# Kernel tuning notes

Measured on AMD Instinct MI355X. Metric: run time of the kernel, lower is better.

## Reference

```python
import jax, jax.numpy as jnp
import numpy as np

B, T, D = 2, 512, 512
UNITS, H = 512, 8
DEPTH = UNITS // H  # 64


def setup_inputs() -> dict:
    key = jax.random.key(0)
    ks = jax.random.split(key, 16)
    s = 0.05  # keras 'random_normal' initializer stddev
    inp = {
        "query": jax.random.normal(ks[0], (B, T, D), jnp.float32),
        "key": jax.random.normal(ks[1], (B, T, D), jnp.float32),
        "value": jax.random.normal(ks[2], (B, T, D), jnp.float32),
        # input projections (Dense(units) with bias)
        "Wq": jax.random.normal(ks[3], (D, UNITS), jnp.float32) * s,
        "bq": jnp.zeros((UNITS,), jnp.float32),
        "Wk": jax.random.normal(ks[4], (D, UNITS), jnp.float32) * s,
        "bk": jnp.zeros((UNITS,), jnp.float32),
        "Wv": jax.random.normal(ks[5], (D, UNITS), jnp.float32) * s,
        "bv": jnp.zeros((UNITS,), jnp.float32),
        # per-head additive-attention params, stacked over heads
        "Wq_h": jax.random.normal(ks[6], (H, DEPTH, DEPTH), jnp.float32) * s,
        "Wk_h": jax.random.normal(ks[7], (H, DEPTH, DEPTH), jnp.float32) * s,
        "va_h": jax.random.normal(ks[8], (H, DEPTH), jnp.float32) * s,
        "b_h": jnp.zeros((H, DEPTH), jnp.float32),
        # output projection
        "Wo": jax.random.normal(ks[9], (UNITS, UNITS), jnp.float32) * s,
        "bo": jnp.zeros((UNITS,), jnp.float32),
    }
    return inp


def _split_heads(x):
    b = x.shape[0]
    return x.reshape(b, -1, H, DEPTH).transpose(0, 2, 1, 3)  # [B,H,T,depth]


def reference(query, key, value, Wq, bq, Wk, bk, Wv, bv,
              Wq_h, Wk_h, va_h, b_h, Wo, bo):
    Q = _split_heads(query @ Wq + bq)  # [B,H,T,d]
    K = _split_heads(key @ Wk + bk)    # [B,H,S,d]
    V = _split_heads(value @ Wv + bv)  # computed but unused, as in original

    # per-head linear maps for additive scores
    q = jnp.einsum("bhtd,hde->bhte", Q, Wq_h)
    k = jnp.einsum("bhsd,hde->bhse", K, Wk_h)
    # Bahdanau additive score: tanh(q_t + k_s + b) . v_a, summed over depth
    feat = jnp.tanh(q[:, :, :, None, :] + k[:, :, None, :, :]
                    + b_h[None, :, None, None, :])  # [B,H,T,S,d]
    score = jnp.einsum("bhtse,he->bhts", feat, va_h)  # [B,H,T,S]
    attn = jax.nn.softmax(score, axis=-1)
    # original multiplies by KEY (not value)
    heads = jnp.einsum("bhts,bhsd->bhtd", attn, K)  # [B,H,T,d]
    merged = heads.transpose(0, 2, 1, 3).reshape(query.shape[0], -1, UNITS)
    return merged @ Wo + bo
```

## Files before the change

### kernel.cpp

```cpp
#include <hip/hip_runtime.h>
#include <hip/hip_bf16.h>

#define T_SEQ 512
#define NH 8
#define DEPTH 64
#define UNITS_ 512
#define SCALE2 2.8853900817779268f
#define LOG2E 1.4426950408889634f

typedef __attribute__((ext_vector_type(8))) short short8;
typedef __attribute__((ext_vector_type(4))) float floatx4;

__global__ __launch_bounds__(256) void qk_head_fused(
    const float* __restrict__ query, const float* __restrict__ key,
    const float* __restrict__ Wq, const float* __restrict__ bq,
    const float* __restrict__ Wk, const float* __restrict__ bk,
    const float* __restrict__ Wq_h, const float* __restrict__ Wk_h,
    const float* __restrict__ bh,
    float* __restrict__ eq, float* __restrict__ ekT,
    __hip_bfloat16* __restrict__ KhT)
{
    __shared__ float S1[64][68];
    __shared__ float S2[64][68];

    const int tid = threadIdx.x;
    const int which = blockIdx.z;
    const int h  = blockIdx.x;
    const int m0 = blockIdx.y * 64;
    const int n0 = h * 64;
    const int b  = m0 >> 9;
    const int t0 = m0 & 511;
    const int bh_i = b * NH + h;

    const float* In   = which ? key : query;
    const float* W    = which ? Wk  : Wq;
    const float* bias = which ? bk  : bq;
    const float* Wp   = (which ? Wk_h : Wq_h) + h * 4096;

    float (*As)[68] = S1;
    float (*Bs)[68] = S2;

    const int arow = tid >> 2;
    const int acol = (tid & 3) * 8;
    const int bkk = tid >> 3;
    const int bn = (tid & 7) * 8;

    const int ti = tid >> 4;
    const int tj = tid & 15;

    const int wrow = tid >> 2;
    const int wcol = (tid & 3) * 16;
    float4 wh0 = *(const float4*)&Wp[wrow * 64 + wcol + 0];
    float4 wh1 = *(const float4*)&Wp[wrow * 64 + wcol + 4];
    float4 wh2 = *(const float4*)&Wp[wrow * 64 + wcol + 8];
    float4 wh3 = *(const float4*)&Wp[wrow * 64 + wcol + 12];

    float4 acc[4];
    acc[0] = acc[1] = acc[2] = acc[3] = make_float4(0.f, 0.f, 0.f, 0.f);

    float4 av0 = *(const float4*)&In[(m0 + arow) * 512 + acol];
    float4 av1 = *(const float4*)&In[(m0 + arow) * 512 + acol + 4];
    float4 bv0 = *(const float4*)&W[bkk * 512 + n0 + bn];
    float4 bv1 = *(const float4*)&W[bkk * 512 + n0 + bn + 4];

    for (int k0 = 0; k0 < 512; k0 += 32) {
        __syncthreads();
        As[acol + 0][arow] = av0.x;
        As[acol + 1][arow] = av0.y;
        As[acol + 2][arow] = av0.z;
        As[acol + 3][arow] = av0.w;
        As[acol + 4][arow] = av1.x;
        As[acol + 5][arow] = av1.y;
        As[acol + 6][arow] = av1.z;
        As[acol + 7][arow] = av1.w;
        *(float4*)&Bs[bkk][bn] = bv0;
        *(float4*)&Bs[bkk][bn + 4] = bv1;
        __syncthreads();
        if (k0 + 32 < 512) {
            av0 = *(const float4*)&In[(m0 + arow) * 512 + k0 + 32 + acol];
            av1 = *(const float4*)&In[(m0 + arow) * 512 + k0 + 32 + acol + 4];
            bv0 = *(const float4*)&W[(k0 + 32 + bkk) * 512 + n0 + bn];
            bv1 = *(const float4*)&W[(k0 + 32 + bkk) * 512 + n0 + bn + 4];
        }
        #pragma unroll
        for (int kk = 0; kk < 32; ++kk) {
            float4 a4 = *(const float4*)&As[kk][4 * ti];
            float4 b4 = *(const float4*)&Bs[kk][4 * tj];
            acc[0].x = fmaf(a4.x, b4.x, acc[0].x);
            acc[0].y = fmaf(a4.x, b4.y, acc[0].y);
            acc[0].z = fmaf(a4.x, b4.z, acc[0].z);
            acc[0].w = fmaf(a4.x, b4.w, acc[0].w);
            acc[1].x = fmaf(a4.y, b4.x, acc[1].x);
            acc[1].y = fmaf(a4.y, b4.y, acc[1].y);
            acc[1].z = fmaf(a4.y, b4.z, acc[1].z);
            acc[1].w = fmaf(a4.y, b4.w, acc[1].w);
            acc[2].x = fmaf(a4.z, b4.x, acc[2].x);
            acc[2].y = fmaf(a4.z, b4.y, acc[2].y);
            acc[2].z = fmaf(a4.z, b4.z, acc[2].z);
            acc[2].w = fmaf(a4.z, b4.w, acc[2].w);
            acc[3].x = fmaf(a4.w, b4.x, acc[3].x);
            acc[3].y = fmaf(a4.w, b4.y, acc[3].y);
            acc[3].z = fmaf(a4.w, b4.z, acc[3].z);
            acc[3].w = fmaf(a4.w, b4.w, acc[3].w);
        }
    }

    float4 bb = *(const float4*)&bias[n0 + 4 * tj];
    __syncthreads();
    *(float4*)&S1[4 * tj + 0][4 * ti] =
        make_float4(acc[0].x + bb.x, acc[1].x + bb.x, acc[2].x + bb.x, acc[3].x + bb.x);
    *(float4*)&S1[4 * tj + 1][4 * ti] =
        make_float4(acc[0].y + bb.y, acc[1].y + bb.y, acc[2].y + bb.y, acc[3].y + bb.y);
    *(float4*)&S1[4 * tj + 2][4 * ti] =
        make_float4(acc[0].z + bb.z, acc[1].z + bb.z, acc[2].z + bb.z, acc[3].z + bb.z);
    *(float4*)&S1[4 * tj + 3][4 * ti] =
        make_float4(acc[0].w + bb.w, acc[1].w + bb.w, acc[2].w + bb.w, acc[3].w + bb.w);
    *(float4*)&S2[wrow][wcol + 0]  = wh0;
    *(float4*)&S2[wrow][wcol + 4]  = wh1;
    *(float4*)&S2[wrow][wcol + 8]  = wh2;
    *(float4*)&S2[wrow][wcol + 12] = wh3;
    __syncthreads();

    float4 qa[4];
    qa[0] = qa[1] = qa[2] = qa[3] = make_float4(0.f, 0.f, 0.f, 0.f);
    #pragma unroll 8
    for (int d = 0; d < 64; ++d) {
        float4 a4 = *(const float4*)&S1[d][4 * ti];
        float4 b4 = *(const float4*)&S2[d][4 * tj];
        qa[0].x = fmaf(a4.x, b4.x, qa[0].x);
        qa[0].y = fmaf(a4.x, b4.y, qa[0].y);
        qa[0].z = fmaf(a4.x, b4.z, qa[0].z);
        qa[0].w = fmaf(a4.x, b4.w, qa[0].w);
        qa[1].x = fmaf(a4.y, b4.x, qa[1].x);
        qa[1].y = fmaf(a4.y, b4.y, qa[1].y);
        qa[1].z = fmaf(a4.y, b4.z, qa[1].z);
        qa[1].w = fmaf(a4.y, b4.w, qa[1].w);
        qa[2].x = fmaf(a4.z, b4.x, qa[2].x);
        qa[2].y = fmaf(a4.z, b4.y, qa[2].y);
        qa[2].z = fmaf(a4.z, b4.z, qa[2].z);
        qa[2].w = fmaf(a4.z, b4.w, qa[2].w);
        qa[3].x = fmaf(a4.w, b4.x, qa[3].x);
        qa[3].y = fmaf(a4.w, b4.y, qa[3].y);
        qa[3].z = fmaf(a4.w, b4.z, qa[3].z);
        qa[3].w = fmaf(a4.w, b4.w, qa[3].w);
    }

    if (which == 0) {
        float* outp = eq + ((size_t)bh_i * 512 + t0) * 64;
        #pragma unroll
        for (int r = 0; r < 4; ++r) {
            float4 o;
            o.x = __builtin_amdgcn_exp2f(SCALE2 * qa[r].x);
            o.y = __builtin_amdgcn_exp2f(SCALE2 * qa[r].y);
            o.z = __builtin_amdgcn_exp2f(SCALE2 * qa[r].z);
            o.w = __builtin_amdgcn_exp2f(SCALE2 * qa[r].w);
            *(float4*)&outp[(4 * ti + r) * 64 + 4 * tj] = o;
        }
        return;
    }

    float4 bhv = *(const float4*)&bh[h * 64 + 4 * tj];
    __syncthreads();
    #pragma unroll
    for (int r = 0; r < 4; ++r) {
        S2[4 * tj + 0][4 * ti + r] = __builtin_amdgcn_exp2f(SCALE2 * (qa[r].x + bhv.x));
        S2[4 * tj + 1][4 * ti + r] = __builtin_amdgcn_exp2f(SCALE2 * (qa[r].y + bhv.y));
        S2[4 * tj + 2][4 * ti + r] = __builtin_amdgcn_exp2f(SCALE2 * (qa[r].z + bhv.z));
        S2[4 * tj + 3][4 * ti + r] = __builtin_amdgcn_exp2f(SCALE2 * (qa[r].w + bhv.w));
    }
    __syncthreads();

    const int dd = tid >> 2;
    const int sc = (tid & 3) * 16;
    float* ekp = ekT + ((size_t)bh_i * 64 + dd) * 512 + t0 + sc;
    #pragma unroll
    for (int c = 0; c < 4; ++c)
        *(float4*)&ekp[4 * c] = *(float4*)&S2[dd][sc + 4 * c];

    __hip_bfloat16* kp = KhT + ((size_t)bh_i * 64 + dd) * 512 + t0 + sc;
    union { short8 v; short s[8]; } pk0, pk1;
    #pragma unroll
    for (int i = 0; i < 8; ++i) {
        __hip_bfloat16 b0 = __hip_bfloat16(S1[dd][sc + i]);
        __hip_bfloat16 b1 = __hip_bfloat16(S1[dd][sc + 8 + i]);
        pk0.s[i] = *(short*)&b0;
        pk1.s[i] = *(short*)&b1;
    }
    *(short8*)kp = pk0.v;
    *(short8*)(kp + 8) = pk1.v;
}

__global__ __launch_bounds__(512, 4) void attn_v2(
    const float* __restrict__ eq, const float* __restrict__ ekT,
    const __hip_bfloat16* __restrict__ KhT, const float* __restrict__ va_h,
    float* __restrict__ merged)
{
    __shared__ __hip_bfloat16 pA[16][520];
    __shared__ float wsum[16][8];

    const int tid = threadIdx.x;
    const int w = tid >> 6;
    const int l = tid & 63;
    const int t0 = blockIdx.x * 16;
    const int h = blockIdx.y;
    const int b = blockIdx.z;
    const int bh_i = b * NH + h;

    const float* eq_p = eq + ((size_t)bh_i * 512 + t0) * 64;
    const float* ekT_p = ekT + (size_t)bh_i * 64 * 512 + tid;
    const float* va_p = va_h + h * 64;

    float acc[16];
    #pragma unroll
    for (int t = 0; t < 16; ++t) acc[t] = 0.f;

    #pragma unroll
    for (int e0 = 0; e0 < 64; e0 += 16) {
        float ekv[16];
        #pragma unroll
        for (int j = 0; j < 16; ++j) ekv[j] = ekT_p[(e0 + j) * 512];
        float nv[16];
        #pragma unroll
        for (int j = 0; j < 16; ++j) nv[j] = -2.0f * va_p[e0 + j];
        #pragma unroll
        for (int t = 0; t < 16; ++t) {
            float a = acc[t];
            #pragma unroll
            for (int q = 0; q < 4; ++q) {
                float4 e4 = *(const float4*)&eq_p[t * 64 + e0 + q * 4];
                a = fmaf(nv[q * 4 + 0], __builtin_amdgcn_rcpf(fmaf(e4.x, ekv[q * 4 + 0], 1.0f)), a);
                a = fmaf(nv[q * 4 + 1], __builtin_amdgcn_rcpf(fmaf(e4.y, ekv[q * 4 + 1], 1.0f)), a);
                a = fmaf(nv[q * 4 + 2], __builtin_amdgcn_rcpf(fmaf(e4.z, ekv[q * 4 + 2], 1.0f)), a);
                a = fmaf(nv[q * 4 + 3], __builtin_amdgcn_rcpf(fmaf(e4.w, ekv[q * 4 + 3], 1.0f)), a);
            }
            acc[t] = a;
        }
    }

    float ev[16];
    #pragma unroll
    for (int t = 0; t < 16; ++t) {
        float s = __builtin_amdgcn_exp2f(acc[t] * LOG2E);
        ev[t] = s;
        #pragma unroll
        for (int off = 32; off > 0; off >>= 1) s += __shfl_xor(s, off, 64);
        if (l == 0) wsum[t][w] = s;
    }
    __syncthreads();
    #pragma unroll
    for (int t = 0; t < 16; ++t) {
        float4 s0 = *(float4*)&wsum[t][0];
        float4 s1 = *(float4*)&wsum[t][4];
        float inv = 1.0f / (((s0.x + s0.y) + (s0.z + s0.w)) + ((s1.x + s1.y) + (s1.z + s1.w)));
        pA[t][tid] = __hip_bfloat16(ev[t] * inv);
    }
    __syncthreads();

    if (w < 4) {
        const __hip_bfloat16* kp = KhT + (size_t)bh_i * 64 * 512
                                   + ((size_t)(w * 16 + (l & 15))) * 512 + (l >> 4) * 8;
        const __hip_bfloat16* ap = &pA[l & 15][(l >> 4) * 8];
        floatx4 oacc = {0.f, 0.f, 0.f, 0.f};
        #pragma unroll
        for (int kt = 0; kt < 16; ++kt) {
            short8 af = *(const short8*)(ap + kt * 32);
            short8 bf = *(const short8*)(kp + kt * 32);
            oacc = __builtin_amdgcn_mfma_f32_16x16x32_bf16(af, bf, oacc, 0, 0, 0);
        }
        const int row = (l >> 4) * 4;
        const int col = w * 16 + (l & 15);
        float* mp = merged + ((size_t)(b * 512 + t0 + row)) * 512 + h * 64 + col;
        #pragma unroll
        for (int r = 0; r < 4; ++r) mp[r * 512] = oacc[r];
    }
}

__global__ __launch_bounds__(256) void gemm_out(
    const float* __restrict__ A, const float* __restrict__ W,
    const float* __restrict__ bias, float* __restrict__ C)
{
    __shared__ float As[32][36];
    __shared__ float Bs[32][68];

    const int tid = threadIdx.x;
    const int n0 = blockIdx.x * 64;
    const int m0 = blockIdx.y * 32;

    const int arow = tid >> 3;
    const int acol = (tid & 7) * 4;
    const int bkk = tid >> 3;
    const int bn = (tid & 7) * 8;

    const int ti = tid >> 4;
    const int tj = tid & 15;

    float4 acc0 = make_float4(0.f, 0.f, 0.f, 0.f);
    float4 acc1 = make_float4(0.f, 0.f, 0.f, 0.f);

    float4 av  = *(const float4*)&A[(m0 + arow) * 512 + acol];
    float4 bv0 = *(const float4*)&W[bkk * 512 + n0 + bn];
    float4 bv1 = *(const float4*)&W[bkk * 512 + n0 + bn + 4];

    for (int k0 = 0; k0 < 512; k0 += 32) {
        __syncthreads();
        As[acol + 0][arow] = av.x;
        As[acol + 1][arow] = av.y;
        As[acol + 2][arow] = av.z;
        As[acol + 3][arow] = av.w;
        *(float4*)&Bs[bkk][bn] = bv0;
        *(float4*)&Bs[bkk][bn + 4] = bv1;
        __syncthreads();
        if (k0 + 32 < 512) {
            av  = *(const float4*)&A[(m0 + arow) * 512 + k0 + 32 + acol];
            bv0 = *(const float4*)&W[(k0 + 32 + bkk) * 512 + n0 + bn];
            bv1 = *(const float4*)&W[(k0 + 32 + bkk) * 512 + n0 + bn + 4];
        }
        #pragma unroll
        for (int kk = 0; kk < 32; ++kk) {
            float2 a2 = *(const float2*)&As[kk][2 * ti];
            float4 b4 = *(const float4*)&Bs[kk][4 * tj];
            acc0.x = fmaf(a2.x, b4.x, acc0.x);
            acc0.y = fmaf(a2.x, b4.y, acc0.y);
            acc0.z = fmaf(a2.x, b4.z, acc0.z);
            acc0.w = fmaf(a2.x, b4.w, acc0.w);
            acc1.x = fmaf(a2.y, b4.x, acc1.x);
            acc1.y = fmaf(a2.y, b4.y, acc1.y);
            acc1.z = fmaf(a2.y, b4.z, acc1.z);
            acc1.w = fmaf(a2.y, b4.w, acc1.w);
        }
    }
    float4 bb = *(const float4*)&bias[n0 + 4 * tj];
    float4 o0, o1;
    o0.x = acc0.x + bb.x; o0.y = acc0.y + bb.y; o0.z = acc0.z + bb.z; o0.w = acc0.w + bb.w;
    o1.x = acc1.x + bb.x; o1.y = acc1.y + bb.y; o1.z = acc1.z + bb.z; o1.w = acc1.w + bb.w;
    *(float4*)&C[(m0 + 2 * ti) * 512 + n0 + 4 * tj] = o0;
    *(float4*)&C[(m0 + 2 * ti + 1) * 512 + n0 + 4 * tj] = o1;
}

extern "C" void kernel_launch(void* const* d_in, const int* in_sizes, int n_in,
                              void* d_out, int out_size, void* d_ws, size_t ws_size,
                              hipStream_t stream) {
    (void)in_sizes; (void)n_in; (void)out_size; (void)ws_size;
    const float* query = (const float*)d_in[0];
    const float* key   = (const float*)d_in[1];
    const float* Wq   = (const float*)d_in[3];
    const float* bq   = (const float*)d_in[4];
    const float* Wk   = (const float*)d_in[5];
    const float* bk   = (const float*)d_in[6];
    const float* Wq_h = (const float*)d_in[9];
    const float* Wk_h = (const float*)d_in[10];
    const float* va_h = (const float*)d_in[11];
    const float* b_h  = (const float*)d_in[12];
    const float* Wo   = (const float*)d_in[13];
    const float* bo   = (const float*)d_in[14];

    float* out = (float*)d_out;
    float* ws = (float*)d_ws;
    const int SZ = 1024 * 512;
    float* eqb     = ws;
    float* ekTb    = eqb + SZ;
    float* mergedb = ekTb + SZ;
    __hip_bfloat16* KhTb = (__hip_bfloat16*)(mergedb + SZ);

    qk_head_fused<<<dim3(8, 16, 2), 256, 0, stream>>>(query, key, Wq, bq, Wk, bk,
                                                      Wq_h, Wk_h, b_h,
                                                      eqb, ekTb, KhTb);
    attn_v2<<<dim3(32, 8, 2), 512, 0, stream>>>(eqb, ekTb, KhTb, va_h, mergedb);
    gemm_out<<<dim3(8, 32, 1), 256, 0, stream>>>(mergedb, Wo, bo, out);
}
```

Measured before the change: 181.8 us.

## Halve tile sizes across all three kernels to launch more blocks

Halves the row tile in the fused QK projection kernel (64 to 32 rows), the query tile in the attention kernel (16 to 8 rows, with a 1D swizzled grid over batch-heads and zero-padded MFMA rows), and the output-column tile in the output GEMM. The aim is to raise block counts so the many CUs on the device are filled, since the earlier grids launched only 256 to 512 blocks. The cost is lower per-thread data reuse, more redundant weight loads, and MFMA work wasted on the padded rows in attention.

```diff
diff --git a/kernel.cpp b/kernel.cpp
--- a/kernel.cpp
+++ b/kernel.cpp
@@ -20,13 +20,13 @@
     float* __restrict__ eq, float* __restrict__ ekT,
     __hip_bfloat16* __restrict__ KhT)
 {
-    __shared__ float S1[64][68];
+    __shared__ float S1[64][36];
     __shared__ float S2[64][68];
 
     const int tid = threadIdx.x;
     const int which = blockIdx.z;
     const int h  = blockIdx.x;
-    const int m0 = blockIdx.y * 64;
+    const int m0 = blockIdx.y * 32;
     const int n0 = h * 64;
     const int b  = m0 >> 9;
     const int t0 = m0 & 511;
@@ -37,11 +37,8 @@
     const float* bias = which ? bk  : bq;
     const float* Wp   = (which ? Wk_h : Wq_h) + h * 4096;
 
-    float (*As)[68] = S1;
-    float (*Bs)[68] = S2;
-
-    const int arow = tid >> 2;
-    const int acol = (tid & 3) * 8;
+    const int arow = tid >> 3;
+    const int acol = (tid & 7) * 4;
     const int bkk = tid >> 3;
     const int bn = (tid & 7) * 8;
 
@@ -55,164 +52,148 @@
     float4 wh2 = *(const float4*)&Wp[wrow * 64 + wcol + 8];
     float4 wh3 = *(const float4*)&Wp[wrow * 64 + wcol + 12];
 
-    float4 acc[4];
-    acc[0] = acc[1] = acc[2] = acc[3] = make_float4(0.f, 0.f, 0.f, 0.f);
-
-    float4 av0 = *(const float4*)&In[(m0 + arow) * 512 + acol];
-    float4 av1 = *(const float4*)&In[(m0 + arow) * 512 + acol + 4];
+    float4 acc0 = make_float4(0.f, 0.f, 0.f, 0.f);
+    float4 acc1 = make_float4(0.f, 0.f, 0.f, 0.f);
+
+    float4 av  = *(const float4*)&In[(m0 + arow) * 512 + acol];
     float4 bv0 = *(const float4*)&W[bkk * 512 + n0 + bn];
     float4 bv1 = *(const float4*)&W[bkk * 512 + n0 + bn + 4];
 
     for (int k0 = 0; k0 < 512; k0 += 32) {
         __syncthreads();
-        As[acol + 0][arow] = av0.x;
-        As[acol + 1][arow] = av0.y;
-        As[acol + 2][arow] = av0.z;
-        As[acol + 3][arow] = av0.w;
-        As[acol + 4][arow] = av1.x;
-        As[acol + 5][arow] = av1.y;
-        As[acol + 6][arow] = av1.z;
-        As[acol + 7][arow] = av1.w;
-        *(float4*)&Bs[bkk][bn] = bv0;
-        *(float4*)&Bs[bkk][bn + 4] = bv1;
+        S1[acol + 0][arow] = av.x;
+        S1[acol + 1][arow] = av.y;
+        S1[acol + 2][arow] = av.z;
+        S1[acol + 3][arow] = av.w;
+        *(float4*)&S2[bkk][bn] = bv0;
+        *(float4*)&S2[bkk][bn + 4] = bv1;
         __syncthreads();
         if (k0 + 32 < 512) {
-            av0 = *(const float4*)&In[(m0 + arow) * 512 + k0 + 32 + acol];
-            av1 = *(const float4*)&In[(m0 + arow) * 512 + k0 + 32 + acol + 4];
+            av  = *(const float4*)&In[(m0 + arow) * 512 + k0 + 32 + acol];
             bv0 = *(const float4*)&W[(k0 + 32 + bkk) * 512 + n0 + bn];
             bv1 = *(const float4*)&W[(k0 + 32 + bkk) * 512 + n0 + bn + 4];
         }
         #pragma unroll
         for (int kk = 0; kk < 32; ++kk) {
-            float4 a4 = *(const float4*)&As[kk][4 * ti];
-            float4 b4 = *(const float4*)&Bs[kk][4 * tj];
-            acc[0].x = fmaf(a4.x, b4.x, acc[0].x);
-            acc[0].y = fmaf(a4.x, b4.y, acc[0].y);
-            acc[0].z = fmaf(a4.x, b4.z, acc[0].z);
-            acc[0].w = fmaf(a4.x, b4.w, acc[0].w);
-            acc[1].x = fmaf(a4.y, b4.x, acc[1].x);
-            acc[1].y = fmaf(a4.y, b4.y, acc[1].y);
-            acc[1].z = fmaf(a4.y, b4.z, acc[1].z);
-            acc[1].w = fmaf(a4.y, b4.w, acc[1].w);
-            acc[2].x = fmaf(a4.z, b4.x, acc[2].x);
-            acc[2].y = fmaf(a4.z, b4.y, acc[2].y);
-            acc[2].z = fmaf(a4.z, b4.z, acc[2].z);
-            acc[2].w = fmaf(a4.z, b4.w, acc[2].w);
-            acc[3].x = fmaf(a4.w, b4.x, acc[3].x);
-            acc[3].y = fmaf(a4.w, b4.y, acc[3].y);
-            acc[3].z = fmaf(a4.w, b4.z, acc[3].z);
-            acc[3].w = fmaf(a4.w, b4.w, acc[3].w);
+            float2 a2 = *(const float2*)&S1[kk][2 * ti];
+            float4 b4 = *(const float4*)&S2[kk][4 * tj];
+            acc0.x = fmaf(a2.x, b4.x, acc0.x);
+            acc0.y = fmaf(a2.x, b4.y, acc0.y);
+            acc0.z = fmaf(a2.x, b4.z, acc0.z);
+            acc0.w = fmaf(a2.x, b4.w, acc0.w);
+            acc1.x = fmaf(a2.y, b4.x, acc1.x);
+            acc1.y = fmaf(a2.y, b4.y, acc1.y);
+            acc1.z = fmaf(a2.y, b4.z, acc1.z);
+            acc1.w = fmaf(a2.y, b4.w, acc1.w);
         }
     }
 
     float4 bb = *(const float4*)&bias[n0 + 4 * tj];
     __syncthreads();
-    *(float4*)&S1[4 * tj + 0][4 * ti] =
-        make_float4(acc[0].x + bb.x, acc[1].x + bb.x, acc[2].x + bb.x, acc[3].x + bb.x);
-    *(float4*)&S1[4 * tj + 1][4 * ti] =
-        make_float4(acc[0].y + bb.y, acc[1].y + bb.y, acc[2].y + bb.y, acc[3].y + bb.y);
-    *(float4*)&S1[4 * tj + 2][4 * ti] =
-        make_float4(acc[0].z + bb.z, acc[1].z + bb.z, acc[2].z + bb.z, acc[3].z + bb.z);
-    *(float4*)&S1[4 * tj + 3][4 * ti] =
-        make_float4(acc[0].w + bb.w, acc[1].w + bb.w, acc[2].w + bb.w, acc[3].w + bb.w);
+    *(float2*)&S1[4 * tj + 0][2 * ti] = make_float2(acc0.x + bb.x, acc1.x + bb.x);
+    *(float2*)&S1[4 * tj + 1][2 * ti] = make_float2(acc0.y + bb.y, acc1.y + bb.y);
+    *(float2*)&S1[4 * tj + 2][2 * ti] = make_float2(acc0.z + bb.z, acc1.z + bb.z);
+    *(float2*)&S1[4 * tj + 3][2 * ti] = make_float2(acc0.w + bb.w, acc1.w + bb.w);
     *(float4*)&S2[wrow][wcol + 0]  = wh0;
     *(float4*)&S2[wrow][wcol + 4]  = wh1;
     *(float4*)&S2[wrow][wcol + 8]  = wh2;
     *(float4*)&S2[wrow][wcol + 12] = wh3;
     __syncthreads();
 
-    float4 qa[4];
-    qa[0] = qa[1] = qa[2] = qa[3] = make_float4(0.f, 0.f, 0.f, 0.f);
-    #pragma unroll 8
+    float4 qa0 = make_float4(0.f, 0.f, 0.f, 0.f);
+    float4 qa1 = make_float4(0.f, 0.f, 0.f, 0.f);
+    #pragma unroll 16
     for (int d = 0; d < 64; ++d) {
-        float4 a4 = *(const float4*)&S1[d][4 * ti];
+        float2 a2 = *(const float2*)&S1[d][2 * ti];
         float4 b4 = *(const float4*)&S2[d][4 * tj];
-        qa[0].x = fmaf(a4.x, b4.x, qa[0].x);
-        qa[0].y = fmaf(a4.x, b4.y, qa[0].y);
-        qa[0].z = fmaf(a4.x, b4.z, qa[0].z);
-        qa[0].w = fmaf(a4.x, b4.w, qa[0].w);
-        qa[1].x = fmaf(a4.y, b4.x, qa[1].x);
-        qa[1].y = fmaf(a4.y, b4.y, qa[1].y);
-        qa[1].z = fmaf(a4.y, b4.z, qa[1].z);
-        qa[1].w = fmaf(a4.y, b4.w, qa[1].w);
-        qa[2].x = fmaf(a4.z, b4.x, qa[2].x);
-        qa[2].y = fmaf(a4.z, b4.y, qa[2].y);
-        qa[2].z = fmaf(a4.z, b4.z, qa[2].z);
-        qa[2].w = fmaf(a4.z, b4.w, qa[2].w);
-        qa[3].x = fmaf(a4.w, b4.x, qa[3].x);
-        qa[3].y = fmaf(a4.w, b4.y, qa[3].y);
-        qa[3].z = fmaf(a4.w, b4.z, qa[3].z);
-        qa[3].w = fmaf(a4.w, b4.w, qa[3].w);
+        qa0.x = fmaf(a2.x, b4.x, qa0.x);
+        qa0.y = fmaf(a2.x, b4.y, qa0.y);
+        qa0.z = fmaf(a2.x, b4.z, qa0.z);
+        qa0.w = fmaf(a2.x, b4.w, qa0.w);
+        qa1.x = fmaf(a2.y, b4.x, qa1.x);
+        qa1.y = fmaf(a2.y, b4.y, qa1.y);
+        qa1.z = fmaf(a2.y, b4.z, qa1.z);
+        qa1.w = fmaf(a2.y, b4.w, qa1.w);
     }
 
     if (which == 0) {
         float* outp = eq + ((size_t)bh_i * 512 + t0) * 64;
-        #pragma unroll
-        for (int r = 0; r < 4; ++r) {
-            float4 o;
-            o.x = __builtin_amdgcn_exp2f(SCALE2 * qa[r].x);
-            o.y = __builtin_amdgcn_exp2f(SCALE2 * qa[r].y);
-            o.z = __builtin_amdgcn_exp2f(SCALE2 * qa[r].z);
-            o.w = __builtin_amdgcn_exp2f(SCALE2 * qa[r].w);
-            *(float4*)&outp[(4 * ti + r) * 64 + 4 * tj] = o;
-        }
+        float4 o0, o1;
+        o0.x = __builtin_amdgcn_exp2f(SCALE2 * qa0.x);
+        o0.y = __builtin_amdgcn_exp2f(SCALE2 * qa0.y);
+        o0.z = __builtin_amdgcn_exp2f(SCALE2 * qa0.z);
+        o0.w = __builtin_amdgcn_exp2f(SCALE2 * qa0.w);
+        o1.x = __builtin_amdgcn_exp2f(SCALE2 * qa1.x);
+        o1.y = __builtin_amdgcn_exp2f(SCALE2 * qa1.y);
+        o1.z = __builtin_amdgcn_exp2f(SCALE2 * qa1.z);
+        o1.w = __builtin_amdgcn_exp2f(SCALE2 * qa1.w);
+        *(float4*)&outp[(2 * ti + 0) * 64 + 4 * tj] = o0;
+        *(float4*)&outp[(2 * ti + 1) * 64 + 4 * tj] = o1;
         return;
     }
 
     float4 bhv = *(const float4*)&bh[h * 64 + 4 * tj];
     __syncthreads();
-    #pragma unroll
-    for (int r = 0; r < 4; ++r) {
-        S2[4 * tj + 0][4 * ti + r] = __builtin_amdgcn_exp2f(SCALE2 * (qa[r].x + bhv.x));
-        S2[4 * tj + 1][4 * ti + r] = __builtin_amdgcn_exp2f(SCALE2 * (qa[r].y + bhv.y));
-        S2[4 * tj + 2][4 * ti + r] = __builtin_amdgcn_exp2f(SCALE2 * (qa[r].z + bhv.z));
-        S2[4 * tj + 3][4 * ti + r] = __builtin_amdgcn_exp2f(SCALE2 * (qa[r].w + bhv.w));
-    }
+    *(float2*)&S2[4 * tj + 0][2 * ti] = make_float2(
+        __builtin_amdgcn_exp2f(SCALE2 * (qa0.x + bhv.x)),
+        __builtin_amdgcn_exp2f(SCALE2 * (qa1.x + bhv.x)));
+    *(float2*)&S2[4 * tj + 1][2 * ti] = make_float2(
+        __builtin_amdgcn_exp2f(SCALE2 * (qa0.y + bhv.y)),
+        __builtin_amdgcn_exp2f(SCALE2 * (qa1.y + bhv.y)));
+    *(float2*)&S2[4 * tj + 2][2 * ti] = make_float2(
+        __builtin_amdgcn_exp2f(SCALE2 * (qa0.z + bhv.z)),
+        __builtin_amdgcn_exp2f(SCALE2 * (qa1.z + bhv.z)));
+    *(float2*)&S2[4 * tj + 3][2 * ti] = make_float2(
+        __builtin_amdgcn_exp2f(SCALE2 * (qa0.w + bhv.w)),
+        __builtin_amdgcn_exp2f(SCALE2 * (qa1.w + bhv.w)));
     __syncthreads();
 
     const int dd = tid >> 2;
-    const int sc = (tid & 3) * 16;
+    const int sc = (tid & 3) * 8;
     float* ekp = ekT + ((size_t)bh_i * 64 + dd) * 512 + t0 + sc;
-    #pragma unroll
-    for (int c = 0; c < 4; ++c)
-        *(float4*)&ekp[4 * c] = *(float4*)&S2[dd][sc + 4 * c];
+    *(float4*)&ekp[0] = *(float4*)&S2[dd][sc];
+    *(float4*)&ekp[4] = *(float4*)&S2[dd][sc + 4];
 
     __hip_bfloat16* kp = KhT + ((size_t)bh_i * 64 + dd) * 512 + t0 + sc;
-    union { short8 v; short s[8]; } pk0, pk1;
+    union { short8 v; short s[8]; } pk;
     #pragma unroll
     for (int i = 0; i < 8; ++i) {
         __hip_bfloat16 b0 = __hip_bfloat16(S1[dd][sc + i]);
-        __hip_bfloat16 b1 = __hip_bfloat16(S1[dd][sc + 8 + i]);
-        pk0.s[i] = *(short*)&b0;
-        pk1.s[i] = *(short*)&b1;
-    }
-    *(short8*)kp = pk0.v;
-    *(short8*)(kp + 8) = pk1.v;
+        pk.s[i] = *(short*)&b0;
+    }
+    *(short8*)kp = pk.v;
 }
 
-__global__ __launch_bounds__(512, 4) void attn_v2(
+__global__ __launch_bounds__(512, 8) void attn_v3(
     const float* __restrict__ eq, const float* __restrict__ ekT,
     const __hip_bfloat16* __restrict__ KhT, const float* __restrict__ va_h,
     float* __restrict__ merged)
 {
     __shared__ __hip_bfloat16 pA[16][520];
-    __shared__ float wsum[16][8];
+    __shared__ float wsum[8][8];
 
     const int tid = threadIdx.x;
     const int w = tid >> 6;
     const int l = tid & 63;
-    const int t0 = blockIdx.x * 16;
-    const int h = blockIdx.y;
-    const int b = blockIdx.z;
-    const int bh_i = b * NH + h;
+    const int bid = blockIdx.x;
+    const int swz = (bid & 7) * 128 + (bid >> 3);
+    const int t0 = (swz & 63) * 8;
+    const int bh_i = swz >> 6;
+    const int h = bh_i & 7;
+    const int b = bh_i >> 3;
+
+    {
+        short8 z = {0, 0, 0, 0, 0, 0, 0, 0};
+        *(short8*)&pA[8 + (tid >> 6)][(tid & 63) * 8] = z;
+    }
 
     const float* eq_p = eq + ((size_t)bh_i * 512 + t0) * 64;
     const float* ekT_p = ekT + (size_t)bh_i * 64 * 512 + tid;
     const float* va_p = va_h + h * 64;
 
-    float acc[16];
-    #pragma unroll
-    for (int t = 0; t < 16; ++t) acc[t] = 0.f;
+    float acc[8];
+    #pragma unroll
+    for (int t = 0; t < 8; ++t) acc[t] = 0.f;
 
     #pragma unroll
     for (int e0 = 0; e0 < 64; e0 += 16) {
@@ -223,7 +204,7 @@
         #pragma unroll
         for (int j = 0; j < 16; ++j) nv[j] = -2.0f * va_p[e0 + j];
         #pragma unroll
-        for (int t = 0; t < 16; ++t) {
+        for (int t = 0; t < 8; ++t) {
             float a = acc[t];
             #pragma unroll
             for (int q = 0; q < 4; ++q) {
@@ -237,9 +218,9 @@
         }
     }
 
-    float ev[16];
-    #pragma unroll
-    for (int t = 0; t < 16; ++t) {
+    float ev[8];
+    #pragma unroll
+    for (int t = 0; t < 8; ++t) {
         float s = __builtin_amdgcn_exp2f(acc[t] * LOG2E);
         ev[t] = s;
         #pragma unroll
@@ -248,7 +229,7 @@
     }
     __syncthreads();
     #pragma unroll
-    for (int t = 0; t < 16; ++t) {
+    for (int t = 0; t < 8; ++t) {
         float4 s0 = *(float4*)&wsum[t][0];
         float4 s1 = *(float4*)&wsum[t][4];
         float inv = 1.0f / (((s0.x + s0.y) + (s0.z + s0.w)) + ((s1.x + s1.y) + (s1.z + s1.w)));
@@ -267,11 +248,13 @@
             short8 bf = *(const short8*)(kp + kt * 32);
             oacc = __builtin_amdgcn_mfma_f32_16x16x32_bf16(af, bf, oacc, 0, 0, 0);
         }
-        const int row = (l >> 4) * 4;
-        const int col = w * 16 + (l & 15);
-        float* mp = merged + ((size_t)(b * 512 + t0 + row)) * 512 + h * 64 + col;
-        #pragma unroll
-        for (int r = 0; r < 4; ++r) mp[r * 512] = oacc[r];
+        if ((l >> 4) < 2) {
+            const int row = (l >> 4) * 4;
+            const int col = w * 16 + (l & 15);
+            float* mp = merged + ((size_t)(b * 512 + t0 + row)) * 512 + h * 64 + col;
+            #pragma unroll
+            for (int r = 0; r < 4; ++r) mp[r * 512] = oacc[r];
+        }
     }
 }
 
@@ -280,26 +263,25 @@
     const float* __restrict__ bias, float* __restrict__ C)
 {
     __shared__ float As[32][36];
-    __shared__ float Bs[32][68];
+    __shared__ float Bs[32][36];
 
     const int tid = threadIdx.x;
-    const int n0 = blockIdx.x * 64;
+    const int n0 = blockIdx.x * 32;
     const int m0 = blockIdx.y * 32;
 
     const int arow = tid >> 3;
     const int acol = (tid & 7) * 4;
     const int bkk = tid >> 3;
-    const int bn = (tid & 7) * 8;
+    const int bn = (tid & 7) * 4;
 
     const int ti = tid >> 4;
     const int tj = tid & 15;
 
-    float4 acc0 = make_float4(0.f, 0.f, 0.f, 0.f);
-    float4 acc1 = make_float4(0.f, 0.f, 0.f, 0.f);
-
-    float4 av  = *(const float4*)&A[(m0 + arow) * 512 + acol];
-    float4 bv0 = *(const float4*)&W[bkk * 512 + n0 + bn];
-    float4 bv1 = *(const float4*)&W[bkk * 512 + n0 + bn + 4];
+    float2 acc0 = make_float2(0.f, 0.f);
+    float2 acc1 = make_float2(0.f, 0.f);
+
+    float4 av = *(const float4*)&A[(m0 + arow) * 512 + acol];
+    float4 bv = *(const float4*)&W[bkk * 512 + n0 + bn];
 
     for (int k0 = 0; k0 < 512; k0 += 32) {
         __syncthreads();
@@ -307,34 +289,27 @@
         As[acol + 1][arow] = av.y;
         As[acol + 2][arow] = av.z;
         As[acol + 3][arow] = av.w;
-        *(float4*)&Bs[bkk][bn] = bv0;
-        *(float4*)&Bs[bkk][bn + 4] = bv1;
+        *(float4*)&Bs[bkk][bn] = bv;
         __syncthreads();
         if (k0 + 32 < 512) {
-            av  = *(const float4*)&A[(m0 + arow) * 512 + k0 + 32 + acol];
-            bv0 = *(const float4*)&W[(k0 + 32 + bkk) * 512 + n0 + bn];
-            bv1 = *(const float4*)&W[(k0 + 32 + bkk) * 512 + n0 + bn + 4];
+            av = *(const float4*)&A[(m0 + arow) * 512 + k0 + 32 + acol];
+            bv = *(const float4*)&W[(k0 + 32 + bkk) * 512 + n0 + bn];
         }
         #pragma unroll
         for (int kk = 0; kk < 32; ++kk) {
             float2 a2 = *(const float2*)&As[kk][2 * ti];
-            float4 b4 = *(const float4*)&Bs[kk][4 * tj];
-            acc0.x = fmaf(a2.x, b4.x, acc0.x);
-            acc0.y = fmaf(a2.x, b4.y, acc0.y);
-            acc0.z = fmaf(a2.x, b4.z, acc0.z);
-            acc0.w = fmaf(a2.x, b4.w, acc0.w);
-            acc1.x = fmaf(a2.y, b4.x, acc1.x);
-            acc1.y = fmaf(a2.y, b4.y, acc1.y);
-            acc1.z = fmaf(a2.y, b4.z, acc1.z);
-            acc1.w = fmaf(a2.y, b4.w, acc1.w);
-        }
-    }
-    float4 bb = *(const float4*)&bias[n0 + 4 * tj];
-    float4 o0, o1;
-    o0.x = acc0.x + bb.x; o0.y = acc0.y + bb.y; o0.z = acc0.z + bb.z; o0.w = acc0.w + bb.w;
-    o1.x = acc1.x + bb.x; o1.y = acc1.y + bb.y; o1.z = acc1.z + bb.z; o1.w = acc1.w + bb.w;
-    *(float4*)&C[(m0 + 2 * ti) * 512 + n0 + 4 * tj] = o0;
-    *(float4*)&C[(m0 + 2 * ti + 1) * 512 + n0 + 4 * tj] = o1;
+            float2 b2 = *(const float2*)&Bs[kk][2 * tj];
+            acc0.x = fmaf(a2.x, b2.x, acc0.x);
+            acc0.y = fmaf(a2.x, b2.y, acc0.y);
+            acc1.x = fmaf(a2.y, b2.x, acc1.x);
+            acc1.y = fmaf(a2.y, b2.y, acc1.y);
+        }
+    }
+    float2 bb = *(const float2*)&bias[n0 + 2 * tj];
+    float2 o0 = make_float2(acc0.x + bb.x, acc0.y + bb.y);
+    float2 o1 = make_float2(acc1.x + bb.x, acc1.y + bb.y);
+    *(float2*)&C[(m0 + 2 * ti + 0) * 512 + n0 + 2 * tj] = o0;
+    *(float2*)&C[(m0 + 2 * ti + 1) * 512 + n0 + 2 * tj] = o1;
 }
 
 extern "C" void kernel_launch(void* const* d_in, const int* in_sizes, int n_in,
@@ -362,9 +337,9 @@
     float* mergedb = ekTb + SZ;
     __hip_bfloat16* KhTb = (__hip_bfloat16*)(mergedb + SZ);
 
-    qk_head_fused<<<dim3(8, 16, 2), 256, 0, stream>>>(query, key, Wq, bq, Wk, bk,
+    qk_head_fused<<<dim3(8, 32, 2), 256, 0, stream>>>(query, key, Wq, bq, Wk, bk,
                                                       Wq_h, Wk_h, b_h,
                                                       eqb, ekTb, KhTb);
-    attn_v2<<<dim3(32, 8, 2), 512, 0, stream>>>(eqb, ekTb, KhTb, va_h, mergedb);
-    gemm_out<<<dim3(8, 32, 1), 256, 0, stream>>>(mergedb, Wo, bo, out);
+    attn_v3<<<dim3(1024, 1, 1), 512, 0, stream>>>(eqb, ekTb, KhTb, va_h, mergedb);
+    gemm_out<<<dim3(16, 32, 1), 256, 0, stream>>>(mergedb, Wo, bo, out);
 }
```

Result: slower. 333.3 us (+83.4%).

## Preload all ekT values per thread, swizzle block order, split score accumulators

Applied to the files above, without the earlier changes.

The attention kernel now loads all 64 ekT values for its key position into registers once, where it previously reloaded them in four chunks. It reads va directly and folds the -2 factor into the exp scale, and splits each score accumulation into two independent FMA chains to shorten dependencies. The grid is flattened to 1D with a swizzle that spreads (b,h) work across XCDs for better L2 locality. The larger register footprint may hurt occupancy under the launch bound of 512 threads with 4 blocks.

```diff
diff --git a/kernel.cpp b/kernel.cpp
--- a/kernel.cpp
+++ b/kernel.cpp
@@ -37,9 +37,6 @@
     const float* bias = which ? bk  : bq;
     const float* Wp   = (which ? Wk_h : Wq_h) + h * 4096;
 
-    float (*As)[68] = S1;
-    float (*Bs)[68] = S2;
-
     const int arow = tid >> 2;
     const int acol = (tid & 3) * 8;
     const int bkk = tid >> 3;
@@ -65,16 +62,16 @@
 
     for (int k0 = 0; k0 < 512; k0 += 32) {
         __syncthreads();
-        As[acol + 0][arow] = av0.x;
-        As[acol + 1][arow] = av0.y;
-        As[acol + 2][arow] = av0.z;
-        As[acol + 3][arow] = av0.w;
-        As[acol + 4][arow] = av1.x;
-        As[acol + 5][arow] = av1.y;
-        As[acol + 6][arow] = av1.z;
-        As[acol + 7][arow] = av1.w;
-        *(float4*)&Bs[bkk][bn] = bv0;
-        *(float4*)&Bs[bkk][bn + 4] = bv1;
+        S1[acol + 0][arow] = av0.x;
+        S1[acol + 1][arow] = av0.y;
+        S1[acol + 2][arow] = av0.z;
+        S1[acol + 3][arow] = av0.w;
+        S1[acol + 4][arow] = av1.x;
+        S1[acol + 5][arow] = av1.y;
+        S1[acol + 6][arow] = av1.z;
+        S1[acol + 7][arow] = av1.w;
+        *(float4*)&S2[bkk][bn] = bv0;
+        *(float4*)&S2[bkk][bn + 4] = bv1;
         __syncthreads();
         if (k0 + 32 < 512) {
             av0 = *(const float4*)&In[(m0 + arow) * 512 + k0 + 32 + acol];
@@ -84,8 +81,8 @@
         }
         #pragma unroll
         for (int kk = 0; kk < 32; ++kk) {
-            float4 a4 = *(const float4*)&As[kk][4 * ti];
-            float4 b4 = *(const float4*)&Bs[kk][4 * tj];
+            float4 a4 = *(const float4*)&S1[kk][4 * ti];
+            float4 b4 = *(const float4*)&S2[kk][4 * tj];
             acc[0].x = fmaf(a4.x, b4.x, acc[0].x);
             acc[0].y = fmaf(a4.x, b4.y, acc[0].y);
             acc[0].z = fmaf(a4.x, b4.z, acc[0].z);
@@ -150,10 +147,11 @@
         #pragma unroll
         for (int r = 0; r < 4; ++r) {
             float4 o;
-            o.x = __builtin_amdgcn_exp2f(SCALE2 * qa[r].x);
-            o.y = __builtin_amdgcn_exp2f(SCALE2 * qa[r].y);
-            o.z = __builtin_amdgcn_exp2f(SCALE2 * qa[r].z);
-            o.w = __builtin_amdgcn_exp2f(SCALE2 * qa[r].w);
+            float4 a = qa[r];
+            o.x = __builtin_amdgcn_exp2f(SCALE2 * a.x);
+            o.y = __builtin_amdgcn_exp2f(SCALE2 * a.y);
+            o.z = __builtin_amdgcn_exp2f(SCALE2 * a.z);
+            o.w = __builtin_amdgcn_exp2f(SCALE2 * a.w);
             *(float4*)&outp[(4 * ti + r) * 64 + 4 * tj] = o;
         }
         return;
@@ -190,7 +188,7 @@
     *(short8*)(kp + 8) = pk1.v;
 }
 
-__global__ __launch_bounds__(512, 4) void attn_v2(
+__global__ __launch_bounds__(512, 4) void attn_v6(
     const float* __restrict__ eq, const float* __restrict__ ekT,
     const __hip_bfloat16* __restrict__ KhT, const float* __restrict__ va_h,
     float* __restrict__ merged)
@@ -201,46 +199,47 @@
     const int tid = threadIdx.x;
     const int w = tid >> 6;
     const int l = tid & 63;
-    const int t0 = blockIdx.x * 16;
-    const int h = blockIdx.y;
-    const int b = blockIdx.z;
-    const int bh_i = b * NH + h;
+    const int bid = blockIdx.x;
+    const int swz = (bid & 7) * 64 + (bid >> 3);
+    const int t0 = (swz & 31) * 16;
+    const int bh_i = swz >> 5;
+    const int h = bh_i & 7;
+    const int b = bh_i >> 3;
 
     const float* eq_p = eq + ((size_t)bh_i * 512 + t0) * 64;
     const float* ekT_p = ekT + (size_t)bh_i * 64 * 512 + tid;
     const float* va_p = va_h + h * 64;
 
+    float ekv[64];
+    #pragma unroll
+    for (int j = 0; j < 64; ++j) ekv[j] = ekT_p[j * 512];
+
     float acc[16];
     #pragma unroll
-    for (int t = 0; t < 16; ++t) acc[t] = 0.f;
-
-    #pragma unroll
-    for (int e0 = 0; e0 < 64; e0 += 16) {
-        float ekv[16];
-        #pragma unroll
-        for (int j = 0; j < 16; ++j) ekv[j] = ekT_p[(e0 + j) * 512];
-        float nv[16];
-        #pragma unroll
-        for (int j = 0; j < 16; ++j) nv[j] = -2.0f * va_p[e0 + j];
-        #pragma unroll
-        for (int t = 0; t < 16; ++t) {
-            float a = acc[t];
-            #pragma unroll
-            for (int q = 0; q < 4; ++q) {
-                float4 e4 = *(const float4*)&eq_p[t * 64 + e0 + q * 4];
-                a = fmaf(nv[q * 4 + 0], __builtin_amdgcn_rcpf(fmaf(e4.x, ekv[q * 4 + 0], 1.0f)), a);
-                a = fmaf(nv[q * 4 + 1], __builtin_amdgcn_rcpf(fmaf(e4.y, ekv[q * 4 + 1], 1.0f)), a);
-                a = fmaf(nv[q * 4 + 2], __builtin_amdgcn_rcpf(fmaf(e4.z, ekv[q * 4 + 2], 1.0f)), a);
-                a = fmaf(nv[q * 4 + 3], __builtin_amdgcn_rcpf(fmaf(e4.w, ekv[q * 4 + 3], 1.0f)), a);
-            }
-            acc[t] = a;
-        }
+    for (int t = 0; t < 16; ++t) {
+        float a0 = 0.f, a1 = 0.f;
+        #pragma unroll
+        for (int q = 0; q < 8; ++q) {
+            float4 e4 = *(const float4*)&eq_p[t * 64 + q * 8];
+            float4 f4 = *(const float4*)&eq_p[t * 64 + q * 8 + 4];
+            float4 v4 = *(const float4*)&va_p[q * 8];
+            float4 u4 = *(const float4*)&va_p[q * 8 + 4];
+            a0 = fmaf(v4.x, __builtin_amdgcn_rcpf(fmaf(e4.x, ekv[q * 8 + 0], 1.0f)), a0);
+            a0 = fmaf(v4.y, __builtin_amdgcn_rcpf(fmaf(e4.y, ekv[q * 8 + 1], 1.0f)), a0);
+            a0 = fmaf(v4.z, __builtin_amdgcn_rcpf(fmaf(e4.z, ekv[q * 8 + 2], 1.0f)), a0);
+            a0 = fmaf(v4.w, __builtin_amdgcn_rcpf(fmaf(e4.w, ekv[q * 8 + 3], 1.0f)), a0);
+            a1 = fmaf(u4.x, __builtin_amdgcn_rcpf(fmaf(f4.x, ekv[q * 8 + 4], 1.0f)), a1);
+            a1 = fmaf(u4.y, __builtin_amdgcn_rcpf(fmaf(f4.y, ekv[q * 8 + 5], 1.0f)), a1);
+            a1 = fmaf(u4.z, __builtin_amdgcn_rcpf(fmaf(f4.z, ekv[q * 8 + 6], 1.0f)), a1);
+            a1 = fmaf(u4.w, __builtin_amdgcn_rcpf(fmaf(f4.w, ekv[q * 8 + 7], 1.0f)), a1);
+        }
+        acc[t] = a0 + a1;
     }
 
     float ev[16];
     #pragma unroll
     for (int t = 0; t < 16; ++t) {
-        float s = __builtin_amdgcn_exp2f(acc[t] * LOG2E);
+        float s = __builtin_amdgcn_exp2f(-SCALE2 * acc[t]);
         ev[t] = s;
         #pragma unroll
         for (int off = 32; off > 0; off >>= 1) s += __shfl_xor(s, off, 64);
@@ -365,6 +364,6 @@
     qk_head_fused<<<dim3(8, 16, 2), 256, 0, stream>>>(query, key, Wq, bq, Wk, bk,
                                                       Wq_h, Wk_h, b_h,
                                                       eqb, ekTb, KhTb);
-    attn_v2<<<dim3(32, 8, 2), 512, 0, stream>>>(eqb, ekTb, KhTb, va_h, mergedb);
+    attn_v6<<<dim3(512, 1, 1), 512, 0, stream>>>(eqb, ekTb, KhTb, va_h, mergedb);
     gemm_out<<<dim3(8, 32, 1), 256, 0, stream>>>(mergedb, Wo, bo, out);
 }
```

Measured after the change: 180.4 us. No clear change (-0.7%).
